# Optimization experiments

Measured on AMD Instinct MI355X. Metric: run time of the kernel, lower is better.

The kernel has to match this reference:

```python
import jax, jax.numpy as jnp
import numpy as np
import math

DIM = 1024
H = 16
DH = DIM // H
B = 2
L = 1024


def setup_inputs() -> dict:
    key = jax.random.key(0)
    ks = jax.random.split(key, 8)
    s = 1.0 / math.sqrt(DIM)
    return {
        "Q": jax.random.normal(ks[0], (B, L, DIM), jnp.float32),
        "K": jax.random.normal(ks[1], (B, L, DIM), jnp.float32),
        "mask_Q": jax.random.bernoulli(ks[2], 0.1, (B, L)),
        "mask_K": jax.random.bernoulli(ks[3], 0.1, (B, L)),
        "Wq": jax.random.normal(ks[4], (DIM, DIM), jnp.float32) * s,
        "Wk": jax.random.normal(ks[5], (DIM, DIM), jnp.float32) * s,
        "Wv": jax.random.normal(ks[6], (DIM, DIM), jnp.float32) * s,
        "Wo": jax.random.normal(ks[7], (DIM, DIM), jnp.float32) * s,
    }


def reference(Q, K, mask_Q, mask_K, Wq, Wk, Wv, Wo):
    # V defaults to K. Masked positions of inputs are zeroed first.
    Qz = jnp.where(mask_Q[:, :, None], 0.0, Q)
    Kz = jnp.where(mask_K[:, :, None], 0.0, K)
    Vz = Kz  # V = K, masked with mask_K

    # Projections (nn.Linear, no bias): y = x @ W.T
    Qp = jnp.einsum('bld,ed->ble', Qz, Wq)
    Kp = jnp.einsum('bld,ed->ble', Kz, Wk)
    Vp = jnp.einsum('bld,ed->ble', Vz, Wv)

    # split heads: [B, L, H, DH] -> per-head attention
    qh = Qp.reshape(B, L, H, DH)
    kh = Kp.reshape(B, L, H, DH)
    vh = Vp.reshape(B, L, H, DH)

    # NOTE: original scales by sqrt(dim) (full dim), not sqrt(dim_split)
    scores = jnp.einsum('bqhd,bkhd->bhqk', qh, kh) / math.sqrt(DIM)

    # outer-product validity mask: valid iff both q and k positions unmasked
    valid = (~mask_Q)[:, None, :, None] & (~mask_K)[:, None, None, :]  # [B,1,Lq,Lk]
    A = jnp.where(valid, scores, -1e38)
    A = jax.nn.softmax(A, axis=-1)
    A = jnp.where(valid, A, 0.0)

    O = jnp.einsum('bhqk,bkhd->bqhd', A, vh).reshape(B, L, DIM)
    # residual uses the PROJECTED Q (Q was reassigned to fc_q(Q) in torch)
    O = Qp + O
    # masked_forward(fc_o, ...): fc_o applied, masked query rows forced to 0
    ff = jax.nn.relu(jnp.where(mask_Q[:, :, None], 0.0, jnp.einsum('bld,ed->ble', O, Wo)))
    O = O + ff
    return O
```

## Files before the change

kernel.cpp:

```cpp
#include <hip/hip_runtime.h>
#include <hip/hip_bf16.h>


#define DEV __device__ __forceinline__

typedef __attribute__((ext_vector_type(8))) short bf16x8;
typedef __attribute__((ext_vector_type(4))) float f32x4;
typedef __hip_bfloat16 bf16;

DEV void glds16(const bf16* g, bf16* s) {
  __builtin_amdgcn_global_load_lds(
      (const __attribute__((address_space(1))) void*)g,
      (__attribute__((address_space(3))) void*)s, 16, 0, 0);
}

DEV unsigned short f2bu(float x) {
  __hip_bfloat16 b = __float2bfloat16(x);
  unsigned short u;
  __builtin_memcpy(&u, &b, 2);
  return u;
}

DEV float bu2f(unsigned short u) {
  unsigned int v = (unsigned int)u << 16;
  float f;
  __builtin_memcpy(&f, &v, 4);
  return f;
}

__global__ __launch_bounds__(256) void cast_all(
    const float* __restrict__ Q, const float* __restrict__ K,
    const unsigned char* __restrict__ mq_raw, const unsigned char* __restrict__ mk_raw,
    const float* __restrict__ W0, const float* __restrict__ W1,
    const float* __restrict__ W2, const float* __restrict__ W3,
    bf16* __restrict__ Qz, bf16* __restrict__ Kz,
    bf16* __restrict__ o0, bf16* __restrict__ o1,
    bf16* __restrict__ o2, bf16* __restrict__ o3,
    unsigned char* __restrict__ mqn,
    unsigned long long* __restrict__ qm64, unsigned long long* __restrict__ km64) {
  __shared__ int cnt;
  const int z = blockIdx.z;
  const int t = threadIdx.x;
  if (z < 2) {
    const float* X = z ? K : Q;
    const unsigned char* raw = z ? mk_raw : mq_raw;
    bf16* out = z ? Kz : Qz;
    if (t == 0) cnt = 0;
    __syncthreads();
    int c = 0;
#pragma unroll
    for (int j = 0; j < 8; ++j) c += (raw[t * 8 + j] != 0);
    atomicAdd(&cnt, c);
    __syncthreads();
    const bool isByte = cnt > 128;
    int i = (blockIdx.x * 256 + t) * 8;
    int row = i >> 10;
    bool masked = isByte ? (raw[row] != 0) : (((const int*)raw)[row] != 0);
    float4 v0 = *(const float4*)&X[i];
    float4 v1 = *(const float4*)&X[i + 4];
    if (masked) {
      v0 = make_float4(0.f, 0.f, 0.f, 0.f);
      v1 = make_float4(0.f, 0.f, 0.f, 0.f);
    }
    *(ushort4*)&out[i] = make_ushort4(f2bu(v0.x), f2bu(v0.y), f2bu(v0.z), f2bu(v0.w));
    *(ushort4*)&out[i + 4] = make_ushort4(f2bu(v1.x), f2bu(v1.y), f2bu(v1.z), f2bu(v1.w));
  } else if (z < 6) {
    if (blockIdx.x >= 512) return;
    const float* X; bf16* out;
    switch (z) {
      case 2: X = W0; out = o0; break;
      case 3: X = W1; out = o1; break;
      case 4: X = W2; out = o2; break;
      default: X = W3; out = o3; break;
    }
    int i = (blockIdx.x * 256 + t) * 8;
    float4 v0 = *(const float4*)&X[i];
    float4 v1 = *(const float4*)&X[i + 4];
    *(ushort4*)&out[i] = make_ushort4(f2bu(v0.x), f2bu(v0.y), f2bu(v0.z), f2bu(v0.w));
    *(ushort4*)&out[i + 4] = make_ushort4(f2bu(v1.x), f2bu(v1.y), f2bu(v1.z), f2bu(v1.w));
  } else {
    if (blockIdx.x != 0) return;
    if (t == 0) cnt = 0;
    __syncthreads();
    int c = 0;
    for (int i = t; i < 2048; i += 256) c += (mq_raw[i] != 0);
    atomicAdd(&cnt, c);
    __syncthreads();
    const bool isByte = cnt > 128;
    for (int i = t; i < 2048; i += 256)
      mqn[i] = isByte ? (mq_raw[i] != 0) : (((const int*)mq_raw)[i] != 0);
    if (t < 64) {
      const unsigned char* src = (t < 32) ? mk_raw : mq_raw;
      int idx = t & 31;
      unsigned long long m = 0;
      for (int j = 0; j < 64; ++j) {
        int pos = idx * 64 + j;
        bool bit = isByte ? (src[pos] != 0) : (((const int*)src)[pos] != 0);
        m |= (unsigned long long)bit << j;
      }
      if (t < 32) km64[idx] = m; else qm64[idx] = m;
    }
  }
}

template <int MI, int NI, typename EPI>
DEV void gemm_core(const bf16* __restrict__ A, const bf16* __restrict__ W,
                   int K, int brow, int bcol, EPI&& epi) {
  __shared__ bf16 As[2 * MI * 512];
  __shared__ bf16 Bs[2 * NI * 2048];
  const int t = threadIdx.x, l = t & 63, w = t >> 6;
  const int rs = l >> 2;
  const int kcol = (l & 3) * 8;

  f32x4 acc[MI][NI];
#pragma unroll
  for (int i = 0; i < MI; i++)
#pragma unroll
    for (int j = 0; j < NI; j++) acc[i][j] = (f32x4){0.f, 0.f, 0.f, 0.f};

  auto stage = [&](int k0, int b_) {
#pragma unroll
    for (int i = 0; i < MI; ++i)
      if ((i & 3) == w)
        glds16(A + (size_t)(brow + i * 16 + rs) * K + k0 + kcol,
               &As[b_ * MI * 512 + i * 512]);
#pragma unroll
    for (int c = 0; c < NI; ++c)
      glds16(W + (size_t)(bcol + (w * NI + c) * 16 + rs) * K + k0 + kcol,
             &Bs[b_ * NI * 2048 + (w * NI + c) * 512]);
  };

  const int aoff0 = (l & 15) * 32 + (l >> 4) * 8;
  const int boff0 = (w * NI * 16 + (l & 15)) * 32 + (l >> 4) * 8;

  stage(0, 0);
  int buf = 0;
  for (int k0 = 0; k0 < K; k0 += 32) {
    __syncthreads();
    if (k0 + 32 < K) stage(k0 + 32, buf ^ 1);
    bf16x8 a[MI], b[NI];
#pragma unroll
    for (int mi = 0; mi < MI; ++mi)
      a[mi] = *(const bf16x8*)&As[buf * MI * 512 + aoff0 + mi * 512];
#pragma unroll
    for (int ni = 0; ni < NI; ++ni)
      b[ni] = *(const bf16x8*)&Bs[buf * NI * 2048 + boff0 + ni * 512];
#pragma unroll
    for (int mi = 0; mi < MI; ++mi)
#pragma unroll
      for (int ni = 0; ni < NI; ++ni)
        acc[mi][ni] = __builtin_amdgcn_mfma_f32_16x16x32_bf16(a[mi], b[ni], acc[mi][ni], 0, 0, 0);
    buf ^= 1;
  }

#pragma unroll
  for (int mi = 0; mi < MI; ++mi)
#pragma unroll
    for (int ni = 0; ni < NI; ++ni)
#pragma unroll
      for (int r = 0; r < 4; ++r) {
        int row = brow + mi * 16 + (l >> 4) * 4 + r;
        int col = bcol + (w * NI + ni) * 16 + (l & 15);
        epi(row, col, acc[mi][ni][r]);
      }
}

__global__ __launch_bounds__(256) void proj_gemm(
    const bf16* __restrict__ Qz, const bf16* __restrict__ Kz,
    const bf16* __restrict__ Wq, const bf16* __restrict__ Wk, const bf16* __restrict__ Wv,
    bf16* __restrict__ Qpb, bf16* __restrict__ Kpb, bf16* __restrict__ Vpb) {
  const int z = blockIdx.z;
  const int brow = blockIdx.x * 64, bcol = blockIdx.y * 128;
  const bf16* A = (z == 0) ? Qz : Kz;
  const bf16* W = (z == 0) ? Wq : ((z == 1) ? Wk : Wv);
  bf16* dst = (z == 0) ? Qpb : ((z == 1) ? Kpb : Vpb);
  const float scale = (z == 0) ? 0.045084220f : 1.0f;
  gemm_core<4, 2>(A, W, 1024, brow, bcol, [&](int row, int col, float v) {
    dst[((size_t)row << 10) + col] = __float2bfloat16(v * scale);
  });
}

__global__ __launch_bounds__(256) void final_gemm(
    const bf16* __restrict__ Ob, const bf16* __restrict__ Wo,
    float* __restrict__ out, const unsigned char* __restrict__ mq) {
  const int brow = blockIdx.x * 64, bcol = blockIdx.y * 64;
  gemm_core<4, 1>(Ob, Wo, 1024, brow, bcol, [&](int row, int col, float v) {
    size_t idx = ((size_t)row << 10) + col;
    float res = bu2f(((const unsigned short*)Ob)[idx]);
    float ff = mq[row] ? 0.f : fmaxf(v, 0.f);
    out[idx] = res + ff;
  });
}

__global__ __launch_bounds__(256) void attn_fused(
    const bf16* __restrict__ Qpb, const bf16* __restrict__ Kpb, const bf16* __restrict__ Vpb,
    const unsigned long long* __restrict__ qm64, const unsigned long long* __restrict__ km64,
    bf16* __restrict__ Ob) {
  __shared__ bf16 Klds[2][64 * 64];
  __shared__ bf16 Vt[64 * 72];

  const int t = threadIdx.x, l = t & 63, w = t >> 6;
  const int q = l & 15, g = l >> 4;
  const int f = blockIdx.x;
  const int bh = (f & 7) + 8 * ((f >> 3) & 3);
  const int qt = f >> 5;
  const int b = bh >> 4, h = bh & 15;
  const size_t bbase = (size_t)b * 1024;

  const int qg = qt * 64 + w * 16 + q;
  const bf16* qptr = Qpb + (bbase + qg) * 1024 + h * 64 + g * 8;
  const bf16x8 qb0 = *(const bf16x8*)qptr;
  const bf16x8 qb1 = *(const bf16x8*)(qptr + 32);

  float psum = 0.f;
  f32x4 oacc[4];
#pragma unroll
  for (int mf = 0; mf < 4; ++mf) oacc[mf] = (f32x4){0.f, 0.f, 0.f, 0.f};

  const int krow_s = l >> 3;
  const int kcol_s = ((l & 7) ^ krow_s) * 8;
  const int vk0 = 2 * (t & 31);
  const int vdc = t >> 5;
  const int vI0 = ((vk0 >> 5) << 5) | (((vk0 >> 2) & 3) << 3) |
                  (((vk0 >> 4) & 1) << 2) | (vk0 & 3);

  union { uint4 v; unsigned short s[8]; } u0, u1;

  auto stageK = [&](int kt_, int b_) {
#pragma unroll
    for (int c = 0; c < 2; ++c) {
      int cw = w * 2 + c;
      glds16(Kpb + (bbase + kt_ * 64 + cw * 8 + krow_s) * 1024 + h * 64 + kcol_s,
             &Klds[b_][cw * 512]);
    }
  };
  auto loadV = [&](int kt_) {
    const bf16* g0 = Vpb + (bbase + kt_ * 64 + vk0) * 1024 + h * 64 + vdc * 8;
    u0.v = *(const uint4*)g0;
    u1.v = *(const uint4*)(g0 + 1024);
  };

  stageK(0, 0);
  loadV(0);
  int buf = 0;

  for (int kt = 0; kt < 16; ++kt) {
    const unsigned long long km = km64[b * 16 + kt];
    const unsigned long long mloc = km >> (4 * g);

    __syncthreads();

#pragma unroll
    for (int j = 0; j < 8; ++j) {
      unsigned int pk = (unsigned int)u0.s[j] | ((unsigned int)u1.s[j] << 16);
      *(unsigned int*)((char*)Vt + (vdc * 8 + j) * 144 + vI0 * 2) = pk;
    }

    f32x4 S[4];
#pragma unroll
    for (int mf = 0; mf < 4; ++mf) {
#pragma unroll
      for (int r = 0; r < 4; ++r)
        S[mf][r] = ((mloc >> (mf * 16 + r)) & 1ull) ? -1e30f : 0.f;
      const int row = mf * 16 + q;
      const int rowb = row * 128;
      const bf16x8 ka0 = *(const bf16x8*)((const char*)&Klds[buf][0] + rowb + ((g ^ (row & 7)) * 16));
      const bf16x8 ka1 = *(const bf16x8*)((const char*)&Klds[buf][0] + rowb + (((g + 4) ^ (row & 7)) * 16));
      S[mf] = __builtin_amdgcn_mfma_f32_16x16x32_bf16(ka0, qb0, S[mf], 0, 0, 0);
      S[mf] = __builtin_amdgcn_mfma_f32_16x16x32_bf16(ka1, qb1, S[mf], 0, 0, 0);
    }

    unsigned int lo[4], hi[4];
#pragma unroll
    for (int mf = 0; mf < 4; ++mf) {
      float p0 = exp2f(S[mf][0]), p1 = exp2f(S[mf][1]);
      float p2 = exp2f(S[mf][2]), p3 = exp2f(S[mf][3]);
      psum += (p0 + p1) + (p2 + p3);
      lo[mf] = (unsigned int)f2bu(p0) | ((unsigned int)f2bu(p1) << 16);
      hi[mf] = (unsigned int)f2bu(p2) | ((unsigned int)f2bu(p3) << 16);
    }

    __syncthreads();

    if (kt < 15) {
      stageK(kt + 1, buf ^ 1);
      loadV(kt + 1);
    }

#pragma unroll
    for (int ks = 0; ks < 2; ++ks) {
      uint4 pw;
      pw.x = lo[2 * ks];
      pw.y = hi[2 * ks];
      pw.z = lo[2 * ks + 1];
      pw.w = hi[2 * ks + 1];
      const bf16x8 pa = __builtin_bit_cast(bf16x8, pw);
#pragma unroll
      for (int mf = 0; mf < 4; ++mf) {
        const bf16x8 va = *(const bf16x8*)((const char*)Vt + (mf * 16 + q) * 144 + ks * 64 + g * 16);
        oacc[mf] = __builtin_amdgcn_mfma_f32_16x16x32_bf16(va, pa, oacc[mf], 0, 0, 0);
      }
    }
    buf ^= 1;
  }

  psum += __shfl_xor(psum, 16);
  psum += __shfl_xor(psum, 32);

  const unsigned long long qm = qm64[b * 16 + qt];
  const bool qvalid = !((qm >> (w * 16 + q)) & 1ull);
  const float inv = (qvalid && psum > 0.f) ? 1.f / psum : 0.f;
  const float RQ = 22.180709777918f;
#pragma unroll
  for (int mf = 0; mf < 4; ++mf) {
    size_t idx = (bbase + qg) * 1024 + h * 64 + mf * 16 + g * 4;
    ushort4 q4 = *(const ushort4*)&Qpb[idx];
    float4 val;
    val.x = bu2f(q4.x) * RQ + oacc[mf][0] * inv;
    val.y = bu2f(q4.y) * RQ + oacc[mf][1] * inv;
    val.z = bu2f(q4.z) * RQ + oacc[mf][2] * inv;
    val.w = bu2f(q4.w) * RQ + oacc[mf][3] * inv;
    *(ushort4*)&Ob[idx] = make_ushort4(f2bu(val.x), f2bu(val.y), f2bu(val.z), f2bu(val.w));
  }
}

extern "C" void kernel_launch(void* const* d_in, const int* in_sizes, int n_in,
                              void* d_out, int out_size, void* d_ws, size_t ws_size,
                              hipStream_t stream) {
  const float* Q = (const float*)d_in[0];
  const float* K = (const float*)d_in[1];
  const unsigned char* mQraw = (const unsigned char*)d_in[2];
  const unsigned char* mKraw = (const unsigned char*)d_in[3];
  const float* Wq = (const float*)d_in[4];
  const float* Wk = (const float*)d_in[5];
  const float* Wv = (const float*)d_in[6];
  const float* Wo = (const float*)d_in[7];
  float* out = (float*)d_out;

  char* ws = (char*)d_ws;
  const size_t MB = 1024 * 1024;
  bf16* Qz  = (bf16*)(ws + 0);
  bf16* Kz  = (bf16*)(ws + 4 * MB);
  bf16* Wqb = (bf16*)(ws + 8 * MB);
  bf16* Wkb = (bf16*)(ws + 10 * MB);
  bf16* Wvb = (bf16*)(ws + 12 * MB);
  bf16* Wob = (bf16*)(ws + 14 * MB);
  bf16* Qpb = (bf16*)(ws + 16 * MB);
  bf16* Kpb = (bf16*)(ws + 20 * MB);
  bf16* Vpb = (bf16*)(ws + 24 * MB);
  bf16* Ob  = (bf16*)(ws + 28 * MB);
  unsigned char* mqn = (unsigned char*)(ws + 32 * MB);
  unsigned long long* km64 = (unsigned long long*)(ws + 32 * MB + 4096);
  unsigned long long* qm64 = km64 + 32;

  dim3 gc(1024, 1, 7);
  cast_all<<<gc, 256, 0, stream>>>(Q, K, mQraw, mKraw, Wq, Wk, Wv, Wo,
                                   Qz, Kz, Wqb, Wkb, Wvb, Wob, mqn, qm64, km64);

  dim3 gp(32, 8, 3);
  proj_gemm<<<gp, 256, 0, stream>>>(Qz, Kz, Wqb, Wkb, Wvb, Qpb, Kpb, Vpb);

  attn_fused<<<512, 256, 0, stream>>>(Qpb, Kpb, Vpb, qm64, km64, Ob);

  dim3 gf(32, 16);
  final_gemm<<<gf, 256, 0, stream>>>(Ob, Wob, out, mqn);
}
```

Before: 95.87 us.

## Write V pre-transposed and swizzled from projection, stage via direct LDS loads

The projection GEMM now writes V in a per-(batch,head,tile) transposed and XOR-swizzled layout. This lets the attention kernel copy each V tile straight into double-buffered LDS with global_load_lds, replacing the register load and per-iteration transpose scatter. It also drops one __syncthreads per iteration and issues the next-tile K/V prefetch earlier. The cost is a scattered 8-byte store pattern in the V projection epilogue and extra LDS for the second V buffer.

```diff
diff --git a/kernel.cpp b/kernel.cpp
--- a/kernel.cpp
+++ b/kernel.cpp
@@ -156,27 +156,40 @@
 #pragma unroll
   for (int mi = 0; mi < MI; ++mi)
 #pragma unroll
-    for (int ni = 0; ni < NI; ++ni)
-#pragma unroll
-      for (int r = 0; r < 4; ++r) {
-        int row = brow + mi * 16 + (l >> 4) * 4 + r;
-        int col = bcol + (w * NI + ni) * 16 + (l & 15);
-        epi(row, col, acc[mi][ni][r]);
-      }
+    for (int ni = 0; ni < NI; ++ni) {
+      int row0 = brow + mi * 16 + (l >> 4) * 4;
+      int col = bcol + (w * NI + ni) * 16 + (l & 15);
+      epi(row0, col, acc[mi][ni]);
+    }
 }
 
 __global__ __launch_bounds__(256) void proj_gemm(
     const bf16* __restrict__ Qz, const bf16* __restrict__ Kz,
     const bf16* __restrict__ Wq, const bf16* __restrict__ Wk, const bf16* __restrict__ Wv,
-    bf16* __restrict__ Qpb, bf16* __restrict__ Kpb, bf16* __restrict__ Vpb) {
+    bf16* __restrict__ Qpb, bf16* __restrict__ Kpb, bf16* __restrict__ VpT) {
   const int z = blockIdx.z;
   const int brow = blockIdx.x * 64, bcol = blockIdx.y * 128;
   const bf16* A = (z == 0) ? Qz : Kz;
   const bf16* W = (z == 0) ? Wq : ((z == 1) ? Wk : Wv);
-  bf16* dst = (z == 0) ? Qpb : ((z == 1) ? Kpb : Vpb);
-  const float scale = (z == 0) ? 0.045084220f : 1.0f;
-  gemm_core<4, 2>(A, W, 1024, brow, bcol, [&](int row, int col, float v) {
-    dst[((size_t)row << 10) + col] = __float2bfloat16(v * scale);
+  gemm_core<4, 2>(A, W, 1024, brow, bcol, [&](int row0, int col, f32x4 v) {
+    if (z == 2) {
+      int b_ = row0 >> 10, tok = row0 & 1023;
+      int hh = col >> 6, dd = col & 63;
+      int tile = tok >> 6, k0 = tok & 63;
+      int I0 = (((k0 >> 5) & 1) << 5) | (((k0 >> 2) & 3) << 3) | (((k0 >> 4) & 1) << 2);
+      size_t base = ((((size_t)(b_ * 16 + hh)) * 16 + tile) << 13) + dd * 128;
+      char* p = (char*)VpT + base + ((I0 * 2) ^ ((dd & 7) << 4));
+      *(ushort4*)p = make_ushort4(f2bu(v[0]), f2bu(v[1]), f2bu(v[2]), f2bu(v[3]));
+    } else if (z == 0) {
+      const float scale = 0.045084220f;
+#pragma unroll
+      for (int r = 0; r < 4; ++r)
+        Qpb[((size_t)(row0 + r) << 10) + col] = __float2bfloat16(v[r] * scale);
+    } else {
+#pragma unroll
+      for (int r = 0; r < 4; ++r)
+        Kpb[((size_t)(row0 + r) << 10) + col] = __float2bfloat16(v[r]);
+    }
   });
 }
 
@@ -184,20 +197,23 @@
     const bf16* __restrict__ Ob, const bf16* __restrict__ Wo,
     float* __restrict__ out, const unsigned char* __restrict__ mq) {
   const int brow = blockIdx.x * 64, bcol = blockIdx.y * 64;
-  gemm_core<4, 1>(Ob, Wo, 1024, brow, bcol, [&](int row, int col, float v) {
-    size_t idx = ((size_t)row << 10) + col;
-    float res = bu2f(((const unsigned short*)Ob)[idx]);
-    float ff = mq[row] ? 0.f : fmaxf(v, 0.f);
-    out[idx] = res + ff;
+  gemm_core<4, 1>(Ob, Wo, 1024, brow, bcol, [&](int row0, int col, f32x4 v) {
+#pragma unroll
+    for (int r = 0; r < 4; ++r) {
+      size_t idx = ((size_t)(row0 + r) << 10) + col;
+      float res = bu2f(((const unsigned short*)Ob)[idx]);
+      float ff = mq[row0 + r] ? 0.f : fmaxf(v[r], 0.f);
+      out[idx] = res + ff;
+    }
   });
 }
 
 __global__ __launch_bounds__(256) void attn_fused(
-    const bf16* __restrict__ Qpb, const bf16* __restrict__ Kpb, const bf16* __restrict__ Vpb,
+    const bf16* __restrict__ Qpb, const bf16* __restrict__ Kpb, const bf16* __restrict__ VpT,
     const unsigned long long* __restrict__ qm64, const unsigned long long* __restrict__ km64,
     bf16* __restrict__ Ob) {
   __shared__ bf16 Klds[2][64 * 64];
-  __shared__ bf16 Vt[64 * 72];
+  __shared__ bf16 Vt[2][64 * 64];
 
   const int t = threadIdx.x, l = t & 63, w = t >> 6;
   const int q = l & 15, g = l >> 4;
@@ -219,12 +235,7 @@
 
   const int krow_s = l >> 3;
   const int kcol_s = ((l & 7) ^ krow_s) * 8;
-  const int vk0 = 2 * (t & 31);
-  const int vdc = t >> 5;
-  const int vI0 = ((vk0 >> 5) << 5) | (((vk0 >> 2) & 3) << 3) |
-                  (((vk0 >> 4) & 1) << 2) | (vk0 & 3);
-
-  union { uint4 v; unsigned short s[8]; } u0, u1;
+  const bf16* vbase = VpT + (((size_t)(b * 16 + h)) << 16);
 
   auto stageK = [&](int kt_, int b_) {
 #pragma unroll
@@ -234,26 +245,24 @@
              &Klds[b_][cw * 512]);
     }
   };
-  auto loadV = [&](int kt_) {
-    const bf16* g0 = Vpb + (bbase + kt_ * 64 + vk0) * 1024 + h * 64 + vdc * 8;
-    u0.v = *(const uint4*)g0;
-    u1.v = *(const uint4*)(g0 + 1024);
+  auto stageV = [&](int kt_, int b_) {
+    const bf16* src = vbase + ((size_t)kt_ << 12);
+    glds16(src + t * 8, &Vt[b_][t * 8]);
+    glds16(src + 2048 + t * 8, &Vt[b_][2048 + t * 8]);
   };
 
   stageK(0, 0);
-  loadV(0);
+  stageV(0, 0);
   int buf = 0;
 
   for (int kt = 0; kt < 16; ++kt) {
-    const unsigned long long km = km64[b * 16 + kt];
-    const unsigned long long mloc = km >> (4 * g);
-
-    __syncthreads();
-
-#pragma unroll
-    for (int j = 0; j < 8; ++j) {
-      unsigned int pk = (unsigned int)u0.s[j] | ((unsigned int)u1.s[j] << 16);
-      *(unsigned int*)((char*)Vt + (vdc * 8 + j) * 144 + vI0 * 2) = pk;
+    const unsigned long long mloc = km64[b * 16 + kt] >> (4 * g);
+
+    __syncthreads();
+
+    if (kt < 15) {
+      stageK(kt + 1, buf ^ 1);
+      stageV(kt + 1, buf ^ 1);
     }
 
     f32x4 S[4];
@@ -280,13 +289,6 @@
       hi[mf] = (unsigned int)f2bu(p2) | ((unsigned int)f2bu(p3) << 16);
     }
 
-    __syncthreads();
-
-    if (kt < 15) {
-      stageK(kt + 1, buf ^ 1);
-      loadV(kt + 1);
-    }
-
 #pragma unroll
     for (int ks = 0; ks < 2; ++ks) {
       uint4 pw;
@@ -297,7 +299,9 @@
       const bf16x8 pa = __builtin_bit_cast(bf16x8, pw);
 #pragma unroll
       for (int mf = 0; mf < 4; ++mf) {
-        const bf16x8 va = *(const bf16x8*)((const char*)Vt + (mf * 16 + q) * 144 + ks * 64 + g * 16);
+        const int vrow = mf * 16 + q;
+        const bf16x8 va = *(const bf16x8*)((const char*)&Vt[buf][0] + vrow * 128 +
+                                           ((ks * 64 + g * 16) ^ ((q & 7) << 4)));
         oacc[mf] = __builtin_amdgcn_mfma_f32_16x16x32_bf16(va, pa, oacc[mf], 0, 0, 0);
       }
     }
@@ -347,7 +351,7 @@
   bf16* Wob = (bf16*)(ws + 14 * MB);
   bf16* Qpb = (bf16*)(ws + 16 * MB);
   bf16* Kpb = (bf16*)(ws + 20 * MB);
-  bf16* Vpb = (bf16*)(ws + 24 * MB);
+  bf16* VpT = (bf16*)(ws + 24 * MB);
   bf16* Ob  = (bf16*)(ws + 28 * MB);
   unsigned char* mqn = (unsigned char*)(ws + 32 * MB);
   unsigned long long* km64 = (unsigned long long*)(ws + 32 * MB + 4096);
@@ -358,9 +362,9 @@
                                    Qz, Kz, Wqb, Wkb, Wvb, Wob, mqn, qm64, km64);
 
   dim3 gp(32, 8, 3);
-  proj_gemm<<<gp, 256, 0, stream>>>(Qz, Kz, Wqb, Wkb, Wvb, Qpb, Kpb, Vpb);
-
-  attn_fused<<<512, 256, 0, stream>>>(Qpb, Kpb, Vpb, qm64, km64, Ob);
+  proj_gemm<<<gp, 256, 0, stream>>>(Qz, Kz, Wqb, Wkb, Wvb, Qpb, Kpb, VpT);
+
+  attn_fused<<<512, 256, 0, stream>>>(Qpb, Kpb, VpT, qm64, km64, Ob);
 
   dim3 gf(32, 16);
   final_gemm<<<gf, 256, 0, stream>>>(Ob, Wob, out, mqn);
```

After: 93.98 us, median of 2. -2.0%, faster.
